# Optimization experiments

Measured on AMD Instinct MI355X. Metric: run time of the kernel, lower is better.

The kernel has to match this reference:

```python
import jax, jax.numpy as jnp
import numpy as np

NUM_AGENTS = 5
B = 512          # graphs in batch
NP = 50          # nodes per graph
N = B * NP
EPG = 400        # edges per graph
E = B * EPG
H, C = 8, 64     # heads, per-head channels
F = H * C        # 512 node feature dim after concat
GRU_IN = 2 * F   # agent emb + graph emb
GRU_H = 128


def _gat_layer(x, src, dst, ea, W, a_src, a_dst, We, ae, b):
    # PyG GATConv: per-edge additive attention with edge features, softmax over dst
    n = x.shape[0]
    h = (x @ W).reshape(n, H, C)                          # [n,H,C]
    al = (h * a_src).sum(-1)[src] + (h * a_dst).sum(-1)[dst] \
         + ((ea @ We).reshape(-1, H, C) * ae).sum(-1)     # [e,H]
    al = jax.nn.leaky_relu(al, 0.2)
    amax = jax.ops.segment_max(al, dst, num_segments=n)
    amax = jnp.where(jnp.isfinite(amax), amax, 0.0)
    p = jnp.exp(al - amax[dst])
    denom = jax.ops.segment_sum(p, dst, num_segments=n)
    alpha = p / (denom[dst] + 1e-16)
    out = jax.ops.segment_sum(alpha[:, :, None] * h[src], dst, num_segments=n)
    return out.reshape(n, F) + b


def _gru(x_seq, h0, Wih, Whh, bih, bhh):
    # torch nn.GRU math, batch_first input [B,T,I]
    def step(h, x_t):
        gi = x_t @ Wih + bih
        gh = h @ Whh + bhh
        ir, iz, inn = jnp.split(gi, 3, axis=-1)
        hr, hz, hn = jnp.split(gh, 3, axis=-1)
        r = jax.nn.sigmoid(ir + hr)
        z = jax.nn.sigmoid(iz + hz)
        n_ = jnp.tanh(inn + r * hn)
        h_new = (1.0 - z) * n_ + z * h
        return h_new, h_new
    h_last, ys = jax.lax.scan(step, h0, jnp.swapaxes(x_seq, 0, 1))
    return jnp.swapaxes(ys, 0, 1), h_last


def _forward(x, edge_index, edge_attr, hidden_state,
             W1, a_src1, a_dst1, We1, ae1, b1,
             W2, a_src2, a_dst2, We2, ae2, b2,
             W3, a_src3, a_dst3, We3, ae3, b3,
             gru_Wih, gru_Whh, gru_bih, gru_bhh,
             fc1_W, fc1_b, fc2_W, fc2_b, log_std):
    src, dst = edge_index[0], edge_index[1]
    # conv1: add_self_loops=False
    x1 = jax.nn.relu(_gat_layer(x, src, dst, edge_attr, W1, a_src1, a_dst1, We1, ae1, b1))
    # conv2/3: add self loops with fill_value='mean' (mean of incoming edge_attr per node)
    cnt = jax.ops.segment_sum(jnp.ones((E,), x.dtype), dst, num_segments=N)
    loop_attr = jax.ops.segment_sum(edge_attr, dst, num_segments=N) / jnp.maximum(cnt, 1.0)[:, None]
    loops = jnp.arange(N, dtype=edge_index.dtype)
    src2 = jnp.concatenate([src, loops])
    dst2 = jnp.concatenate([dst, loops])
    ea2 = jnp.concatenate([edge_attr, loop_attr], axis=0)
    x2 = jax.nn.relu(_gat_layer(x1, src2, dst2, ea2, W2, a_src2, a_dst2, We2, ae2, b2))
    x3 = jax.nn.relu(_gat_layer(x2, src2, dst2, ea2, W3, a_src3, a_dst3, We3, ae3, b3))
    # global mean pool (each graph has NP nodes, contiguous)
    batch = jnp.repeat(jnp.arange(B), NP)
    graph_emb = jax.ops.segment_sum(x3, batch, num_segments=B) / NP   # [B,F]
    # first NUM_AGENTS nodes of each graph
    agent_idx = (jnp.arange(B)[:, None] * NP + jnp.arange(NUM_AGENTS)).reshape(-1)
    agent_emb = x3[agent_idx]                                          # [B*A,F]
    graph_rep = jnp.repeat(graph_emb, NUM_AGENTS, axis=0)
    combined = jnp.concatenate([agent_emb, graph_rep], axis=1).reshape(B, NUM_AGENTS, GRU_IN)
    gru_out, h_last = _gru(combined, hidden_state[0], gru_Wih, gru_Whh, gru_bih, gru_bhh)
    f1 = jax.nn.relu(gru_out.reshape(-1, GRU_H) @ fc1_W + fc1_b)
    action_mean = (f1 @ fc2_W + fc2_b).reshape(B, NUM_AGENTS, -1)
    action_std = jnp.broadcast_to(jnp.exp(jnp.clip(log_std, -20.0, 2.0)), action_mean.shape)
    return action_mean, action_std, h_last[None]


def setup_inputs() -> dict:
    ks = jax.random.split(jax.random.key(0), 24)
    rng = np.random.default_rng(0)
    # random edges within each graph, no self-loops
    src_l = rng.integers(0, NP, size=(B, EPG))
    dst_l = (src_l + 1 + rng.integers(0, NP - 1, size=(B, EPG))) % NP
    off = (np.arange(B) * NP)[:, None]
    edge_index = jnp.asarray(np.stack([(src_l + off).reshape(-1), (dst_l + off).reshape(-1)]), dtype=jnp.int32)

    def p(k, shape, fan):
        return jax.random.normal(k, shape, jnp.float32) / float(np.sqrt(fan))

    z = lambda *s: jnp.zeros(s, jnp.float32)
    return {
        "x": jax.random.normal(ks[0], (N, 4), jnp.float32),
        "edge_index": edge_index,
        "edge_attr": jax.random.uniform(ks[1], (E, 1), jnp.float32),
        "hidden_state": z(1, B, GRU_H),
        "W1": p(ks[2], (4, F), 4), "a_src1": p(ks[3], (H, C), C), "a_dst1": p(ks[4], (H, C), C),
        "We1": p(ks[5], (1, F), 1), "ae1": p(ks[6], (H, C), C), "b1": z(F),
        "W2": p(ks[7], (F, F), F), "a_src2": p(ks[8], (H, C), C), "a_dst2": p(ks[9], (H, C), C),
        "We2": p(ks[10], (1, F), 1), "ae2": p(ks[11], (H, C), C), "b2": z(F),
        "W3": p(ks[12], (F, F), F), "a_src3": p(ks[13], (H, C), C), "a_dst3": p(ks[14], (H, C), C),
        "We3": p(ks[15], (1, F), 1), "ae3": p(ks[16], (H, C), C), "b3": z(F),
        "gru_Wih": p(ks[17], (GRU_IN, 3 * GRU_H), GRU_IN),
        "gru_Whh": p(ks[18], (GRU_H, 3 * GRU_H), GRU_H),
        "gru_bih": z(3 * GRU_H), "gru_bhh": z(3 * GRU_H),
        "fc1_W": p(ks[19], (GRU_H, 64), GRU_H), "fc1_b": z(64),
        "fc2_W": p(ks[20], (64, 3), 64), "fc2_b": z(3),
        "log_std": jnp.full((1, 1, 3), -1.6, jnp.float32),
    }


def reference(x, edge_index, edge_attr, hidden_state,
              W1, a_src1, a_dst1, We1, ae1, b1,
              W2, a_src2, a_dst2, We2, ae2, b2,
              W3, a_src3, a_dst3, We3, ae3, b3,
              gru_Wih, gru_Whh, gru_bih, gru_bhh,
              fc1_W, fc1_b, fc2_W, fc2_b, log_std):
    return _forward(x, edge_index, edge_attr, hidden_state,
                    W1, a_src1, a_dst1, We1, ae1, b1,
                    W2, a_src2, a_dst2, We2, ae2, b2,
                    W3, a_src3, a_dst3, We3, ae3, b3,
                    gru_Wih, gru_Whh, gru_bih, gru_bhh,
                    fc1_W, fc1_b, fc2_W, fc2_b, log_std)
```

## Files before the change

### kernel.cpp

```cpp
#include <hip/hip_runtime.h>
#include <math.h>

#define NN 25600
#define BB 512
#define NP 50
#define EPG 400
#define EE 204800
#define HH 8
#define CC 64
#define FF 512
#define GRUH 128
#define GRUIN 1024
#define NTP 25664

typedef unsigned short ushort_t;
typedef __attribute__((ext_vector_type(8))) short bf16x8;
typedef __attribute__((ext_vector_type(4))) float f32x4;

__device__ __forceinline__ float wave_reduce_sum(float v) {
  #pragma unroll
  for (int m = 32; m >= 1; m >>= 1) v += __shfl_xor(v, m, 64);
  return v;
}

__device__ __forceinline__ ushort_t f2bf(float x) {
  union { float f; unsigned int u; } v; v.f = x;
  unsigned int r = v.u + 0x7fffu + ((v.u >> 16) & 1u);
  return (ushort_t)(r >> 16);
}

__device__ __forceinline__ float bf2f(ushort_t u) {
  union { unsigned int u; float f; } v; v.u = ((unsigned int)u) << 16;
  return v.f;
}

__device__ __forceinline__ void gload_lds16(const ushort_t* g, ushort_t* l) {
  __builtin_amdgcn_global_load_lds(
      (const __attribute__((address_space(1))) void*)g,
      (__attribute__((address_space(3))) void*)l, 16, 0, 0);
}

__global__ void k_wedot(const float* __restrict__ We1, const float* __restrict__ ae1,
                        const float* __restrict__ We2, const float* __restrict__ ae2,
                        const float* __restrict__ We3, const float* __restrict__ ae3,
                        float* __restrict__ wdot) {
  const float* We = blockIdx.x == 0 ? We1 : (blockIdx.x == 1 ? We2 : We3);
  const float* ae = blockIdx.x == 0 ? ae1 : (blockIdx.x == 1 ? ae2 : ae3);
  int head = threadIdx.x >> 6, lane = threadIdx.x & 63;
  float v = We[head * 64 + lane] * ae[head * 64 + lane];
  v = wave_reduce_sum(v);
  if (lane == 0) wdot[blockIdx.x * 8 + head] = v;
}

__global__ void k_lattr(const int* __restrict__ ei, const float* __restrict__ eattr,
                        float* __restrict__ lattr, float* __restrict__ gmm) {
  int g = blockIdx.x, tid = threadIdx.x;
  __shared__ float esum[NP];
  __shared__ int cnt[NP];
  __shared__ unsigned int mn, mx;
  if (tid < NP) { esum[tid] = 0.f; cnt[tid] = 0; }
  if (tid == 0) { mn = 0x7f7fffffu; mx = 0u; }
  __syncthreads();
  for (int e = tid; e < EPG; e += 256) {
    int ge = g * EPG + e;
    int d = ei[EE + ge] - g * NP;
    float a = eattr[ge];
    atomicAdd(&esum[d], a);
    atomicAdd(&cnt[d], 1);
    atomicMax(&mx, __float_as_uint(a));
    atomicMin(&mn, __float_as_uint(a));
  }
  __syncthreads();
  if (tid < NP) {
    float la = esum[tid] / (float)max(cnt[tid], 1);
    lattr[g * NP + tid] = la;
    atomicMax(&mx, __float_as_uint(la));
    atomicMin(&mn, __float_as_uint(la));
  }
  __syncthreads();
  if (tid == 0) { gmm[g * 2] = __uint_as_float(mn); gmm[g * 2 + 1] = __uint_as_float(mx); }
}

__global__ __launch_bounds__(256) void k_cvt_t(const float* __restrict__ W,
                                               ushort_t* __restrict__ Wt,
                                               int K, int N) {
  __shared__ float t[32][33];
  int n0 = blockIdx.x * 32, k0 = blockIdx.y * 32;
  int tx = threadIdx.x & 31, ty = threadIdx.x >> 5;
  #pragma unroll
  for (int i = 0; i < 4; i++)
    t[ty + i * 8][tx] = W[(size_t)(k0 + ty + i * 8) * N + n0 + tx];
  __syncthreads();
  #pragma unroll
  for (int i = 0; i < 4; i++)
    Wt[(size_t)(n0 + ty + i * 8) * K + k0 + tx] = f2bf(t[tx][ty + i * 8]);
}

__global__ __launch_bounds__(256) void k_bgemmT(
    const ushort_t* __restrict__ Wt, const ushort_t* __restrict__ X,
    const float* __restrict__ a_src, const float* __restrict__ a_dst,
    ushort_t* __restrict__ hT, float* __restrict__ ssg, float* __restrict__ sdg) {
  __shared__ ushort_t As[128 * 32];
  __shared__ ushort_t Bs[128 * 32];
  int tid = threadIdx.x;
  int w = tid >> 6, l = tid & 63;
  int row0 = blockIdx.y * 128;
  int col0 = blockIdx.x * 128;
  int wr = w >> 1, wc = w & 1;

  f32x4 acc[4][4];
  #pragma unroll
  for (int i = 0; i < 4; i++)
    #pragma unroll
    for (int j = 0; j < 4; j++) acc[i][j] = (f32x4){0.f, 0.f, 0.f, 0.f};

  int srow = w * 32 + (l >> 2);
  int skcol = (l & 3) * 8;
  const ushort_t* Ag = Wt + (size_t)(row0 + srow) * FF + skcol;
  const ushort_t* Bg = X + (size_t)(col0 + srow) * FF + skcol;
  ushort_t* AsW = &As[w * 1024];
  ushort_t* BsW = &Bs[w * 1024];

  int m_l = l & 15, kq = (l >> 4) * 8;
  const ushort_t* ArdA = &As[(wr * 64 + m_l) * 32 + kq];
  const ushort_t* BrdB = &Bs[(wc * 64 + m_l) * 32 + kq];

  for (int k0 = 0; k0 < FF; k0 += 32) {
    gload_lds16(Ag + k0, AsW);
    gload_lds16(Ag + (size_t)16 * FF + k0, AsW + 512);
    gload_lds16(Bg + k0, BsW);
    gload_lds16(Bg + (size_t)16 * FF + k0, BsW + 512);
    __syncthreads();
    bf16x8 af[4], bfr[4];
    #pragma unroll
    for (int t = 0; t < 4; t++) {
      af[t]  = *(const bf16x8*)(ArdA + t * 16 * 32);
      bfr[t] = *(const bf16x8*)(BrdB + t * 16 * 32);
    }
    #pragma unroll
    for (int mt = 0; mt < 4; mt++)
      #pragma unroll
      for (int nt = 0; nt < 4; nt++)
        acc[mt][nt] = __builtin_amdgcn_mfma_f32_16x16x32_bf16(af[mt], bfr[nt], acc[mt][nt], 0, 0, 0);
    __syncthreads();
  }

  int head = (row0 + wr * 64) >> 6;
  int rq = (l >> 4) * 4, cl = l & 15;
  float ds[4] = {0.f, 0.f, 0.f, 0.f}, dd[4] = {0.f, 0.f, 0.f, 0.f};
  #pragma unroll
  for (int mt = 0; mt < 4; mt++) {
    #pragma unroll
    for (int r = 0; r < 4; r++) {
      int f = row0 + wr * 64 + mt * 16 + rq + r;
      float a_s = a_src[f], a_d = a_dst[f];
      #pragma unroll
      for (int nt = 0; nt < 4; nt++) {
        float v = acc[mt][nt][r];
        ds[nt] += v * a_s;
        dd[nt] += v * a_d;
        int n = col0 + wc * 64 + nt * 16 + cl;
        hT[(size_t)f * NTP + n] = f2bf(v);
      }
    }
  }
  #pragma unroll
  for (int nt = 0; nt < 4; nt++) {
    ds[nt] += __shfl_xor(ds[nt], 16, 64); ds[nt] += __shfl_xor(ds[nt], 32, 64);
    dd[nt] += __shfl_xor(dd[nt], 16, 64); dd[nt] += __shfl_xor(dd[nt], 32, 64);
  }
  if (l < 16) {
    #pragma unroll
    for (int nt = 0; nt < 4; nt++) {
      int n = col0 + wc * 64 + nt * 16 + l;
      ssg[(size_t)n * 8 + head] = ds[nt];
      sdg[(size_t)n * 8 + head] = dd[nt];
    }
  }
}

__global__ __launch_bounds__(256) void k_gatm(
    const ushort_t* __restrict__ hT,
    const float* __restrict__ xin, const float* __restrict__ W1,
    ushort_t* __restrict__ xout,
    const float* __restrict__ a_src, const float* __restrict__ a_dst,
    const float* __restrict__ ssg, const float* __restrict__ sdg,
    const int* __restrict__ ei, const float* __restrict__ eattr,
    const float* __restrict__ lattr, const float* __restrict__ gmm,
    const float* __restrict__ wdot_all, const float* __restrict__ bias,
    int layer, int self_loops) {
  int g = blockIdx.x, hd = blockIdx.y, tid = threadIdx.x;
  int w = tid >> 6, lane = tid & 63;
  const bool l1 = (W1 != nullptr);

  __shared__ __align__(16) ushort_t ht[64 * 72];
  __shared__ __align__(16) float P[50 * 68];
  __shared__ __align__(16) ushort_t Am[64 * 72];
  __shared__ __align__(16) ushort_t ab[16 * 72];
  __shared__ float ssl[64], sdl[64], lat[64];

  float wdot = wdot_all[layer * 8 + hd];
  float minEA = gmm[g * 2], maxEA = gmm[g * 2 + 1];
  float cmax = fmaxf(wdot * maxEA, wdot * minEA);
  if (tid < NP) lat[tid] = lattr[g * NP + tid];
  int m_l = lane & 15, kq8 = (lane >> 4) * 8;

  if (l1) {
    if (tid < 64) ab[tid] = f2bf(a_src[hd * 64 + tid]);
    else if (tid < 128) ab[72 + (tid - 64)] = f2bf(a_dst[hd * 64 + (tid - 64)]);
    { uint4* z = (uint4*)ht; uint4 zz = make_uint4(0u, 0u, 0u, 0u);
      for (int i = tid; i < 576; i += 256) z[i] = zz; }
    float w1c0 = W1[hd * 64 + lane], w1c1 = W1[512 + hd * 64 + lane],
          w1c2 = W1[1024 + hd * 64 + lane], w1c3 = W1[1536 + hd * 64 + lane];
    __syncthreads();
    ushort_t* hrow = (ushort_t*)P;
    #pragma unroll
    for (int i = 0; i < 13; i++) {
      int s = w + 4 * i;
      if (s < NP) {
        const float4 xv = *(const float4*)(xin + (size_t)(g * NP + s) * 4);
        float hv = xv.x * w1c0 + xv.y * w1c1 + xv.z * w1c2 + xv.w * w1c3;
        ushort_t hb = f2bf(hv);
        hrow[s * 72 + lane] = hb;
        ht[lane * 72 + (s ^ (lane & 56))] = hb;
      }
    }
    __syncthreads();
    { int s0 = w * 16;
      f32x4 dacc = (f32x4){0.f, 0.f, 0.f, 0.f};
      #pragma unroll
      for (int kc = 0; kc < 2; kc++) {
        bf16x8 a = *(const bf16x8*)(&ab[m_l * 72 + kc * 32 + kq8]);
        bf16x8 b = *(const bf16x8*)(&hrow[(s0 + m_l) * 72 + kc * 32 + kq8]);
        dacc = __builtin_amdgcn_mfma_f32_16x16x32_bf16(a, b, dacc, 0, 0, 0);
      }
      if (lane < 16) { ssl[s0 + lane] = dacc[0]; sdl[s0 + lane] = dacc[1]; }
    }
    __syncthreads();
    if (tid >= NP && tid < 64) { ssl[tid] = -1e30f; sdl[tid] = 0.f; }
  } else {
    for (int i = tid; i < 2048; i += 256) {
      int c = i >> 5, q = i & 31;
      *(unsigned int*)(&ht[c * 72 + q * 2]) =
          *(const unsigned int*)(&hT[(size_t)(hd * 64 + c) * NTP + g * NP + q * 2]);
    }
    if (tid < 64) {
      ssl[tid] = (tid < NP) ? ssg[(size_t)(g * NP + tid) * 8 + hd] : -1e30f;
      sdl[tid] = (tid < NP) ? sdg[(size_t)(g * NP + tid) * 8 + hd] : 0.f;
    }
  }
  { uint4* z = (uint4*)P; uint4 zz = make_uint4(0u, 0u, 0u, 0u);
    for (int i = tid; i < 850; i += 256) z[i] = zz; }
  __syncthreads();

  float mv = ssl[lane];
  #pragma unroll
  for (int m = 32; m >= 1; m >>= 1) mv = fmaxf(mv, __shfl_xor(mv, m, 64));

  for (int e = tid; e < EPG; e += 256) {
    int eg = g * EPG + e;
    int s = ei[eg] - g * NP;
    int d = ei[EE + eg] - g * NP;
    float al = ssl[s] + sdl[d] + eattr[eg] * wdot;
    al = al > 0.f ? al : 0.2f * al;
    float ub = mv + sdl[d] + cmax;
    ub = ub > 0.f ? ub : 0.2f * ub;
    atomicAdd(&P[d * 68 + s], __expf(al - ub));
  }
  if (self_loops && tid < NP) {
    int d = tid;
    float al = ssl[d] + sdl[d] + lat[d] * wdot;
    al = al > 0.f ? al : 0.2f * al;
    float ub = mv + sdl[d] + cmax;
    ub = ub > 0.f ? ub : 0.2f * ub;
    atomicAdd(&P[d * 68 + d], __expf(al - ub));
  }
  __syncthreads();

  { int d = tid >> 2, part = tid & 3;
    if (d < NP) {
      f32x4 v0 = *(const f32x4*)(&P[d * 68 + part * 16 + 0]);
      f32x4 v1 = *(const f32x4*)(&P[d * 68 + part * 16 + 4]);
      f32x4 v2 = *(const f32x4*)(&P[d * 68 + part * 16 + 8]);
      f32x4 v3 = *(const f32x4*)(&P[d * 68 + part * 16 + 12]);
      float sm = (v0[0] + v0[1] + v0[2] + v0[3]) + (v1[0] + v1[1] + v1[2] + v1[3])
               + (v2[0] + v2[1] + v2[2] + v2[3]) + (v3[0] + v3[1] + v3[2] + v3[3]);
      sm += __shfl_xor(sm, 1, 64);
      sm += __shfl_xor(sm, 2, 64);
      float inv = 1.f / (sm + 1e-16f);
      union { ushort_t u[8]; uint4 q; } p0, p1;
      p0.u[0] = f2bf(v0[0] * inv); p0.u[1] = f2bf(v0[1] * inv);
      p0.u[2] = f2bf(v0[2] * inv); p0.u[3] = f2bf(v0[3] * inv);
      p0.u[4] = f2bf(v1[0] * inv); p0.u[5] = f2bf(v1[1] * inv);
      p0.u[6] = f2bf(v1[2] * inv); p0.u[7] = f2bf(v1[3] * inv);
      p1.u[0] = f2bf(v2[0] * inv); p1.u[1] = f2bf(v2[1] * inv);
      p1.u[2] = f2bf(v2[2] * inv); p1.u[3] = f2bf(v2[3] * inv);
      p1.u[4] = f2bf(v3[0] * inv); p1.u[5] = f2bf(v3[1] * inv);
      p1.u[6] = f2bf(v3[2] * inv); p1.u[7] = f2bf(v3[3] * inv);
      *(uint4*)(&Am[d * 72 + part * 16]) = p0.q;
      *(uint4*)(&Am[d * 72 + part * 16 + 8]) = p1.q;
    } else {
      uint4 zz = make_uint4(0u, 0u, 0u, 0u);
      *(uint4*)(&Am[d * 72 + part * 16]) = zz;
      *(uint4*)(&Am[d * 72 + part * 16 + 8]) = zz;
    }
  }
  __syncthreads();

  int d0 = w * 16;
  f32x4 acc[4];
  #pragma unroll
  for (int ct = 0; ct < 4; ct++) acc[ct] = (f32x4){0.f, 0.f, 0.f, 0.f};
  #pragma unroll
  for (int kc = 0; kc < 2; kc++) {
    int kb = kc * 32 + kq8;
    bf16x8 bfrag = *(const bf16x8*)(&Am[(d0 + m_l) * 72 + kb]);
    #pragma unroll
    for (int ct = 0; ct < 4; ct++) {
      int m = ct * 16 + m_l;
      int ka = l1 ? (kb ^ (m & 56)) : kb;
      bf16x8 afrag = *(const bf16x8*)(&ht[m * 72 + ka]);
      acc[ct] = __builtin_amdgcn_mfma_f32_16x16x32_bf16(afrag, bfrag, acc[ct], 0, 0, 0);
    }
  }

  int d = d0 + m_l, rq = (lane >> 4) * 4;
  if (d < NP) {
    #pragma unroll
    for (int ct = 0; ct < 4; ct++) {
      int cb = ct * 16 + rq;
      const float4 bv = *(const float4*)(&bias[hd * 64 + cb]);
      union { ushort_t u[4]; uint2 v; } pk;
      pk.u[0] = f2bf(fmaxf(acc[ct][0] + bv.x, 0.f));
      pk.u[1] = f2bf(fmaxf(acc[ct][1] + bv.y, 0.f));
      pk.u[2] = f2bf(fmaxf(acc[ct][2] + bv.z, 0.f));
      pk.u[3] = f2bf(fmaxf(acc[ct][3] + bv.w, 0.f));
      *(uint2*)(&xout[(size_t)(g * NP + d) * FF + hd * 64 + cb]) = pk.v;
    }
  }
}

__global__ __launch_bounds__(256) void k_bgemm(
    const ushort_t* __restrict__ A, const ushort_t* __restrict__ Bt,
    const float* __restrict__ bias, float* __restrict__ C,
    int M, int N, int K) {
  __shared__ ushort_t As[128 * 32];
  __shared__ ushort_t Bs[128 * 32];
  int tid = threadIdx.x;
  int w = tid >> 6, l = tid & 63;
  int row0 = blockIdx.y * 128, col0 = blockIdx.x * 128;
  int wr = w >> 1, wc = w & 1;

  f32x4 acc[4][4];
  #pragma unroll
  for (int i = 0; i < 4; i++)
    #pragma unroll
    for (int j = 0; j < 4; j++) acc[i][j] = (f32x4){0.f, 0.f, 0.f, 0.f};

  int srow = w * 32 + (l >> 2);
  int skcol = (l & 3) * 8;
  const ushort_t* Ag = A + (size_t)(row0 + srow) * K + skcol;
  const ushort_t* Bg = Bt + (size_t)(col0 + srow) * K + skcol;
  ushort_t* AsW = &As[w * 1024];
  ushort_t* BsW = &Bs[w * 1024];

  int m_l = l & 15, kq = (l >> 4) * 8;
  const ushort_t* ArdA = &As[(wr * 64 + m_l) * 32 + kq];
  const ushort_t* BrdB = &Bs[(wc * 64 + m_l) * 32 + kq];

  for (int k0 = 0; k0 < K; k0 += 32) {
    gload_lds16(Ag + k0, AsW);
    gload_lds16(Ag + (size_t)16 * K + k0, AsW + 512);
    gload_lds16(Bg + k0, BsW);
    gload_lds16(Bg + (size_t)16 * K + k0, BsW + 512);
    __syncthreads();
    bf16x8 af[4], bfr[4];
    #pragma unroll
    for (int t = 0; t < 4; t++) {
      af[t]  = *(const bf16x8*)(ArdA + t * 16 * 32);
      bfr[t] = *(const bf16x8*)(BrdB + t * 16 * 32);
    }
    #pragma unroll
    for (int mt = 0; mt < 4; mt++)
      #pragma unroll
      for (int nt = 0; nt < 4; nt++)
        acc[mt][nt] = __builtin_amdgcn_mfma_f32_16x16x32_bf16(af[mt], bfr[nt], acc[mt][nt], 0, 0, 0);
    __syncthreads();
  }

  int cl = l & 15, rq = (l >> 4) * 4;
  #pragma unroll
  for (int mt = 0; mt < 4; mt++) {
    #pragma unroll
    for (int nt = 0; nt < 4; nt++) {
      int col = col0 + wc * 64 + nt * 16 + cl;
      float bv = bias ? bias[col] : 0.f;
      #pragma unroll
      for (int r = 0; r < 4; r++) {
        int row = row0 + wr * 64 + mt * 16 + rq + r;
        C[(size_t)row * N + col] = acc[mt][nt][r] + bv;
      }
    }
  }
}

__global__ void k_pool(const ushort_t* __restrict__ x3, ushort_t* __restrict__ combined) {
  int b = blockIdx.x, tid = threadIdx.x;
  float a0 = 0.f, a1 = 0.f;
  for (int n = 0; n < NP; n++) {
    const ushort_t* r = x3 + (size_t)(b * NP + n) * FF;
    a0 += bf2f(r[tid]); a1 += bf2f(r[tid + 256]);
  }
  a0 *= (1.f / NP); a1 *= (1.f / NP);
  ushort_t b0 = f2bf(a0), b1v = f2bf(a1);
  for (int t = 0; t < 5; t++) {
    ushort_t* cb = combined + (size_t)(b * 5 + t) * GRUIN;
    const ushort_t* ag = x3 + (size_t)(b * NP + t) * FF;
    cb[tid] = ag[tid];
    cb[tid + 256] = ag[tid + 256];
    cb[512 + tid] = b0;
    cb[768 + tid] = b1v;
  }
}

__global__ void k_gru(const float* __restrict__ gi_all, const float* __restrict__ h0,
                      const float* __restrict__ Whh, const float* __restrict__ bhh,
                      float* __restrict__ gru_out, float* __restrict__ hlast) {
  int b = blockIdx.x, tid = threadIdx.x;
  __shared__ float hl[GRUH];
  __shared__ float ghb[384];
  if (tid < GRUH) hl[tid] = h0[b * GRUH + tid];
  for (int t = 0; t < 5; t++) {
    __syncthreads();
    float acc = bhh[tid];
    for (int k = 0; k < GRUH; k++) acc += hl[k] * Whh[k * 384 + tid];
    ghb[tid] = acc;
    __syncthreads();
    if (tid < GRUH) {
      const float* gi = gi_all + (size_t)(b * 5 + t) * 384;
      float r = 1.f / (1.f + expf(-(gi[tid] + ghb[tid])));
      float z = 1.f / (1.f + expf(-(gi[128 + tid] + ghb[128 + tid])));
      float nn = tanhf(gi[256 + tid] + r * ghb[256 + tid]);
      float hn = (1.f - z) * nn + z * hl[tid];
      gru_out[(size_t)(b * 5 + t) * GRUH + tid] = hn;
      hl[tid] = hn;
    }
  }
  __syncthreads();
  if (tid < GRUH) hlast[b * GRUH + tid] = hl[tid];
}

__global__ void k_fc(const float* __restrict__ gru_out, const float* __restrict__ fc1W,
                     const float* __restrict__ fc1b, const float* __restrict__ fc2W,
                     const float* __restrict__ fc2b, const float* __restrict__ log_std,
                     float* __restrict__ dout) {
  int row = blockIdx.x, tid = threadIdx.x;
  __shared__ float gbuf[GRUH];
  __shared__ float f1[64];
  gbuf[tid] = gru_out[(size_t)row * GRUH + tid];
  gbuf[tid + 64] = gru_out[(size_t)row * GRUH + 64 + tid];
  __syncthreads();
  float acc = fc1b[tid];
  for (int k = 0; k < GRUH; k++) acc += gbuf[k] * fc1W[k * 64 + tid];
  f1[tid] = fmaxf(acc, 0.f);
  __syncthreads();
  if (tid < 3) {
    float o = fc2b[tid];
    for (int j = 0; j < 64; j++) o += f1[j] * fc2W[j * 3 + tid];
    dout[row * 3 + tid] = o;
    float ls = log_std[tid];
    ls = fminf(fmaxf(ls, -20.f), 2.f);
    dout[7680 + row * 3 + tid] = expf(ls);
  }
}

extern "C" void kernel_launch(void* const* d_in, const int* in_sizes, int n_in,
                              void* d_out, int out_size, void* d_ws, size_t ws_size,
                              hipStream_t stream) {
  const float* x      = (const float*)d_in[0];
  const int*   ei     = (const int*)d_in[1];
  const float* eattr  = (const float*)d_in[2];
  const float* hstate = (const float*)d_in[3];
  const float* W1  = (const float*)d_in[4];
  const float* as1 = (const float*)d_in[5];
  const float* ad1 = (const float*)d_in[6];
  const float* We1 = (const float*)d_in[7];
  const float* ae1 = (const float*)d_in[8];
  const float* b1  = (const float*)d_in[9];
  const float* W2  = (const float*)d_in[10];
  const float* as2 = (const float*)d_in[11];
  const float* ad2 = (const float*)d_in[12];
  const float* We2 = (const float*)d_in[13];
  const float* ae2 = (const float*)d_in[14];
  const float* b2  = (const float*)d_in[15];
  const float* W3  = (const float*)d_in[16];
  const float* as3 = (const float*)d_in[17];
  const float* ad3 = (const float*)d_in[18];
  const float* We3 = (const float*)d_in[19];
  const float* ae3 = (const float*)d_in[20];
  const float* b3  = (const float*)d_in[21];
  const float* Wih = (const float*)d_in[22];
  const float* Whh = (const float*)d_in[23];
  const float* bih = (const float*)d_in[24];
  const float* bhh = (const float*)d_in[25];
  const float* fc1W = (const float*)d_in[26];
  const float* fc1b = (const float*)d_in[27];
  const float* fc2W = (const float*)d_in[28];
  const float* fc2b = (const float*)d_in[29];
  const float* lstd = (const float*)d_in[30];

  float* ws = (float*)d_ws;
  ushort_t* xbf = (ushort_t*)ws;
  ushort_t* hT  = (ushort_t*)(ws + 6553600);
  float* p = ws + 6553600 + 6569984;
  float* ssg   = p;           p += 204800;
  float* sdg   = p;           p += 204800;
  float* lattr = p;           p += 25600;
  float* gmm   = p;           p += 1024;
  float* wdot  = p;           p += 32;
  ushort_t* w2t  = (ushort_t*)p;  p += 131072;
  ushort_t* w3t  = (ushort_t*)p;  p += 131072;
  ushort_t* wiht = (ushort_t*)p;  p += 196608;
  ushort_t* cbf  = (ushort_t*)p;  p += 1310720;
  float* gi_all  = p;         p += 983040;
  float* gru_out = p;         p += 327680;
  float* dout = (float*)d_out;

  k_wedot<<<3, 512, 0, stream>>>(We1, ae1, We2, ae2, We3, ae3, wdot);
  k_lattr<<<BB, 256, 0, stream>>>(ei, eattr, lattr, gmm);
  k_cvt_t<<<dim3(16, 16), 256, 0, stream>>>(W2, w2t, FF, FF);
  k_cvt_t<<<dim3(16, 16), 256, 0, stream>>>(W3, w3t, FF, FF);
  k_cvt_t<<<dim3(12, 32), 256, 0, stream>>>(Wih, wiht, GRUIN, 384);

  k_gatm<<<dim3(BB, HH), 256, 0, stream>>>(nullptr, x, W1, xbf, as1, ad1,
                                           nullptr, nullptr, ei, eattr,
                                           lattr, gmm, wdot, b1, 0, 0);
  k_bgemmT<<<dim3(200, 4), 256, 0, stream>>>(w2t, xbf, as2, ad2, hT, ssg, sdg);
  k_gatm<<<dim3(BB, HH), 256, 0, stream>>>(hT, nullptr, nullptr, xbf, nullptr, nullptr,
                                           ssg, sdg, ei, eattr,
                                           lattr, gmm, wdot, b2, 1, 1);
  k_bgemmT<<<dim3(200, 4), 256, 0, stream>>>(w3t, xbf, as3, ad3, hT, ssg, sdg);
  k_gatm<<<dim3(BB, HH), 256, 0, stream>>>(hT, nullptr, nullptr, xbf, nullptr, nullptr,
                                           ssg, sdg, ei, eattr,
                                           lattr, gmm, wdot, b3, 2, 1);

  k_pool<<<BB, 256, 0, stream>>>(xbf, cbf);
  k_bgemm<<<dim3(3, 20), 256, 0, stream>>>(cbf, wiht, bih, gi_all, 2560, 384, GRUIN);

  k_gru<<<BB, 384, 0, stream>>>(gi_all, hstate, Whh, bhh, gru_out, dout + 15360);
  k_fc<<<2560, 64, 0, stream>>>(gru_out, fc1W, fc1b, fc2W, fc2b, lstd, dout);
}
```

Baseline: 364.7 us.

## Fuse mean-pool and combine into last GAT layer; precompute layer-1 projection separately

The mean-pool and combine step (k_pool) is folded into the epilogue of the third GAT kernel. It sums node outputs per graph with wave shuffles and LDS, then writes the agent rows and the pooled mean straight into the GRU input buffer, so the x3 layer output is never written out and read back. Layer 1's tiny 4-dim projection and its attention scores move to a new k_h1T kernel. That kernel writes the transposed bf16 hT layout, and the attention scores come from W1·a vectors precomputed in k_wedot. This lets all three GAT launches share one code path without the swizzle and MFMA branch, at the cost of an extra launch and hT traffic for layer 1.

```diff
diff --git a/kernel.cpp b/kernel.cpp
--- a/kernel.cpp
+++ b/kernel.cpp
@@ -29,11 +29,6 @@
   return (ushort_t)(r >> 16);
 }
 
-__device__ __forceinline__ float bf2f(ushort_t u) {
-  union { unsigned int u; float f; } v; v.u = ((unsigned int)u) << 16;
-  return v.f;
-}
-
 __device__ __forceinline__ void gload_lds16(const ushort_t* g, ushort_t* l) {
   __builtin_amdgcn_global_load_lds(
       (const __attribute__((address_space(1))) void*)g,
@@ -43,13 +38,26 @@
 __global__ void k_wedot(const float* __restrict__ We1, const float* __restrict__ ae1,
                         const float* __restrict__ We2, const float* __restrict__ ae2,
                         const float* __restrict__ We3, const float* __restrict__ ae3,
-                        float* __restrict__ wdot) {
-  const float* We = blockIdx.x == 0 ? We1 : (blockIdx.x == 1 ? We2 : We3);
-  const float* ae = blockIdx.x == 0 ? ae1 : (blockIdx.x == 1 ? ae2 : ae3);
+                        const float* __restrict__ W1, const float* __restrict__ as1,
+                        const float* __restrict__ ad1,
+                        float* __restrict__ wdot, float* __restrict__ wa) {
   int head = threadIdx.x >> 6, lane = threadIdx.x & 63;
-  float v = We[head * 64 + lane] * ae[head * 64 + lane];
-  v = wave_reduce_sum(v);
-  if (lane == 0) wdot[blockIdx.x * 8 + head] = v;
+  if (blockIdx.x < 3) {
+    const float* We = blockIdx.x == 0 ? We1 : (blockIdx.x == 1 ? We2 : We3);
+    const float* ae = blockIdx.x == 0 ? ae1 : (blockIdx.x == 1 ? ae2 : ae3);
+    float v = We[head * 64 + lane] * ae[head * 64 + lane];
+    v = wave_reduce_sum(v);
+    if (lane == 0) wdot[blockIdx.x * 8 + head] = v;
+  } else {
+    float as = as1[head * 64 + lane], ad = ad1[head * 64 + lane];
+    #pragma unroll
+    for (int k = 0; k < 4; k++) {
+      float wv = W1[k * 512 + head * 64 + lane];
+      float s = wave_reduce_sum(wv * as);
+      float d = wave_reduce_sum(wv * ad);
+      if (lane == 0) { wa[k * 8 + head] = s; wa[32 + k * 8 + head] = d; }
+    }
+  }
 }
 
 __global__ void k_lattr(const int* __restrict__ ei, const float* __restrict__ eattr,
@@ -94,6 +102,31 @@
   #pragma unroll
   for (int i = 0; i < 4; i++)
     Wt[(size_t)(n0 + ty + i * 8) * K + k0 + tx] = f2bf(t[tx][ty + i * 8]);
+}
+
+__global__ __launch_bounds__(256) void k_h1T(
+    const float* __restrict__ x, const float* __restrict__ W1,
+    const float* __restrict__ wa, ushort_t* __restrict__ hT,
+    float* __restrict__ ssg, float* __restrict__ sdg) {
+  int hd = blockIdx.y, tid = threadIdx.x;
+  int n = blockIdx.x * 512 + tid * 2;
+  const float4 x0 = *(const float4*)(x + (size_t)n * 4);
+  const float4 x1 = *(const float4*)(x + (size_t)(n + 1) * 4);
+  float s0 = x0.x * wa[hd] + x0.y * wa[8 + hd] + x0.z * wa[16 + hd] + x0.w * wa[24 + hd];
+  float s1 = x1.x * wa[hd] + x1.y * wa[8 + hd] + x1.z * wa[16 + hd] + x1.w * wa[24 + hd];
+  float d0 = x0.x * wa[32 + hd] + x0.y * wa[40 + hd] + x0.z * wa[48 + hd] + x0.w * wa[56 + hd];
+  float d1 = x1.x * wa[32 + hd] + x1.y * wa[40 + hd] + x1.z * wa[48 + hd] + x1.w * wa[56 + hd];
+  ssg[(size_t)n * 8 + hd] = s0; ssg[(size_t)(n + 1) * 8 + hd] = s1;
+  sdg[(size_t)n * 8 + hd] = d0; sdg[(size_t)(n + 1) * 8 + hd] = d1;
+  #pragma unroll 4
+  for (int fi = 0; fi < 64; fi++) {
+    int f = hd * 64 + fi;
+    float w0 = W1[f], w1 = W1[512 + f], w2 = W1[1024 + f], w3 = W1[1536 + f];
+    float h0 = x0.x * w0 + x0.y * w1 + x0.z * w2 + x0.w * w3;
+    float h1 = x1.x * w0 + x1.y * w1 + x1.z * w2 + x1.w * w3;
+    unsigned int pk = (unsigned int)f2bf(h0) | ((unsigned int)f2bf(h1) << 16);
+    *(unsigned int*)(&hT[(size_t)f * NTP + n]) = pk;
+  }
 }
 
 __global__ __launch_bounds__(256) void k_bgemmT(
@@ -181,9 +214,8 @@
 
 __global__ __launch_bounds__(256) void k_gatm(
     const ushort_t* __restrict__ hT,
-    const float* __restrict__ xin, const float* __restrict__ W1,
     ushort_t* __restrict__ xout,
-    const float* __restrict__ a_src, const float* __restrict__ a_dst,
+    ushort_t* __restrict__ cbf,
     const float* __restrict__ ssg, const float* __restrict__ sdg,
     const int* __restrict__ ei, const float* __restrict__ eattr,
     const float* __restrict__ lattr, const float* __restrict__ gmm,
@@ -191,63 +223,26 @@
     int layer, int self_loops) {
   int g = blockIdx.x, hd = blockIdx.y, tid = threadIdx.x;
   int w = tid >> 6, lane = tid & 63;
-  const bool l1 = (W1 != nullptr);
 
   __shared__ __align__(16) ushort_t ht[64 * 72];
   __shared__ __align__(16) float P[50 * 68];
   __shared__ __align__(16) ushort_t Am[64 * 72];
-  __shared__ __align__(16) ushort_t ab[16 * 72];
-  __shared__ float ssl[64], sdl[64], lat[64];
+  __shared__ float ssl[64], sdl[64];
+  __shared__ float gsum[4 * 64];
 
   float wdot = wdot_all[layer * 8 + hd];
   float minEA = gmm[g * 2], maxEA = gmm[g * 2 + 1];
   float cmax = fmaxf(wdot * maxEA, wdot * minEA);
-  if (tid < NP) lat[tid] = lattr[g * NP + tid];
   int m_l = lane & 15, kq8 = (lane >> 4) * 8;
 
-  if (l1) {
-    if (tid < 64) ab[tid] = f2bf(a_src[hd * 64 + tid]);
-    else if (tid < 128) ab[72 + (tid - 64)] = f2bf(a_dst[hd * 64 + (tid - 64)]);
-    { uint4* z = (uint4*)ht; uint4 zz = make_uint4(0u, 0u, 0u, 0u);
-      for (int i = tid; i < 576; i += 256) z[i] = zz; }
-    float w1c0 = W1[hd * 64 + lane], w1c1 = W1[512 + hd * 64 + lane],
-          w1c2 = W1[1024 + hd * 64 + lane], w1c3 = W1[1536 + hd * 64 + lane];
-    __syncthreads();
-    ushort_t* hrow = (ushort_t*)P;
-    #pragma unroll
-    for (int i = 0; i < 13; i++) {
-      int s = w + 4 * i;
-      if (s < NP) {
-        const float4 xv = *(const float4*)(xin + (size_t)(g * NP + s) * 4);
-        float hv = xv.x * w1c0 + xv.y * w1c1 + xv.z * w1c2 + xv.w * w1c3;
-        ushort_t hb = f2bf(hv);
-        hrow[s * 72 + lane] = hb;
-        ht[lane * 72 + (s ^ (lane & 56))] = hb;
-      }
-    }
-    __syncthreads();
-    { int s0 = w * 16;
-      f32x4 dacc = (f32x4){0.f, 0.f, 0.f, 0.f};
-      #pragma unroll
-      for (int kc = 0; kc < 2; kc++) {
-        bf16x8 a = *(const bf16x8*)(&ab[m_l * 72 + kc * 32 + kq8]);
-        bf16x8 b = *(const bf16x8*)(&hrow[(s0 + m_l) * 72 + kc * 32 + kq8]);
-        dacc = __builtin_amdgcn_mfma_f32_16x16x32_bf16(a, b, dacc, 0, 0, 0);
-      }
-      if (lane < 16) { ssl[s0 + lane] = dacc[0]; sdl[s0 + lane] = dacc[1]; }
-    }
-    __syncthreads();
-    if (tid >= NP && tid < 64) { ssl[tid] = -1e30f; sdl[tid] = 0.f; }
-  } else {
-    for (int i = tid; i < 2048; i += 256) {
-      int c = i >> 5, q = i & 31;
-      *(unsigned int*)(&ht[c * 72 + q * 2]) =
-          *(const unsigned int*)(&hT[(size_t)(hd * 64 + c) * NTP + g * NP + q * 2]);
-    }
-    if (tid < 64) {
-      ssl[tid] = (tid < NP) ? ssg[(size_t)(g * NP + tid) * 8 + hd] : -1e30f;
-      sdl[tid] = (tid < NP) ? sdg[(size_t)(g * NP + tid) * 8 + hd] : 0.f;
-    }
+  for (int i = tid; i < 2048; i += 256) {
+    int c = i >> 5, q = i & 31;
+    *(unsigned int*)(&ht[c * 72 + q * 2]) =
+        *(const unsigned int*)(&hT[(size_t)(hd * 64 + c) * NTP + g * NP + q * 2]);
+  }
+  if (tid < 64) {
+    ssl[tid] = (tid < NP) ? ssg[(size_t)(g * NP + tid) * 8 + hd] : -1e30f;
+    sdl[tid] = (tid < NP) ? sdg[(size_t)(g * NP + tid) * 8 + hd] : 0.f;
   }
   { uint4* z = (uint4*)P; uint4 zz = make_uint4(0u, 0u, 0u, 0u);
     for (int i = tid; i < 850; i += 256) z[i] = zz; }
@@ -269,7 +264,7 @@
   }
   if (self_loops && tid < NP) {
     int d = tid;
-    float al = ssl[d] + sdl[d] + lat[d] * wdot;
+    float al = ssl[d] + sdl[d] + lattr[g * NP + d] * wdot;
     al = al > 0.f ? al : 0.2f * al;
     float ub = mv + sdl[d] + cmax;
     ub = ub > 0.f ? ub : 0.2f * ub;
@@ -317,25 +312,60 @@
     bf16x8 bfrag = *(const bf16x8*)(&Am[(d0 + m_l) * 72 + kb]);
     #pragma unroll
     for (int ct = 0; ct < 4; ct++) {
-      int m = ct * 16 + m_l;
-      int ka = l1 ? (kb ^ (m & 56)) : kb;
-      bf16x8 afrag = *(const bf16x8*)(&ht[m * 72 + ka]);
+      bf16x8 afrag = *(const bf16x8*)(&ht[(ct * 16 + m_l) * 72 + kb]);
       acc[ct] = __builtin_amdgcn_mfma_f32_16x16x32_bf16(afrag, bfrag, acc[ct], 0, 0, 0);
     }
   }
 
   int d = d0 + m_l, rq = (lane >> 4) * 4;
-  if (d < NP) {
+  bool valid = (d < NP);
+  float vv[4][4];
+  #pragma unroll
+  for (int ct = 0; ct < 4; ct++) {
+    const float4 bv = *(const float4*)(&bias[hd * 64 + ct * 16 + rq]);
+    vv[ct][0] = fmaxf(acc[ct][0] + bv.x, 0.f);
+    vv[ct][1] = fmaxf(acc[ct][1] + bv.y, 0.f);
+    vv[ct][2] = fmaxf(acc[ct][2] + bv.z, 0.f);
+    vv[ct][3] = fmaxf(acc[ct][3] + bv.w, 0.f);
+  }
+
+  if (cbf == nullptr) {
+    if (valid) {
+      #pragma unroll
+      for (int ct = 0; ct < 4; ct++) {
+        union { ushort_t u[4]; uint2 v; } pk;
+        pk.u[0] = f2bf(vv[ct][0]); pk.u[1] = f2bf(vv[ct][1]);
+        pk.u[2] = f2bf(vv[ct][2]); pk.u[3] = f2bf(vv[ct][3]);
+        *(uint2*)(&xout[(size_t)(g * NP + d) * FF + hd * 64 + ct * 16 + rq]) = pk.v;
+      }
+    }
+  } else {
     #pragma unroll
     for (int ct = 0; ct < 4; ct++) {
-      int cb = ct * 16 + rq;
-      const float4 bv = *(const float4*)(&bias[hd * 64 + cb]);
-      union { ushort_t u[4]; uint2 v; } pk;
-      pk.u[0] = f2bf(fmaxf(acc[ct][0] + bv.x, 0.f));
-      pk.u[1] = f2bf(fmaxf(acc[ct][1] + bv.y, 0.f));
-      pk.u[2] = f2bf(fmaxf(acc[ct][2] + bv.z, 0.f));
-      pk.u[3] = f2bf(fmaxf(acc[ct][3] + bv.w, 0.f));
-      *(uint2*)(&xout[(size_t)(g * NP + d) * FF + hd * 64 + cb]) = pk.v;
+      #pragma unroll
+      for (int r = 0; r < 4; r++) {
+        float t = valid ? vv[ct][r] : 0.f;
+        t += __shfl_xor(t, 1, 64); t += __shfl_xor(t, 2, 64);
+        t += __shfl_xor(t, 4, 64); t += __shfl_xor(t, 8, 64);
+        if (m_l == 0) gsum[w * 64 + ct * 16 + rq + r] = t;
+      }
+    }
+    if (w == 0 && m_l < 5) {
+      #pragma unroll
+      for (int ct = 0; ct < 4; ct++) {
+        union { ushort_t u[4]; uint2 v; } pk;
+        pk.u[0] = f2bf(vv[ct][0]); pk.u[1] = f2bf(vv[ct][1]);
+        pk.u[2] = f2bf(vv[ct][2]); pk.u[3] = f2bf(vv[ct][3]);
+        *(uint2*)(&cbf[(size_t)(g * 5 + d) * GRUIN + hd * 64 + ct * 16 + rq]) = pk.v;
+      }
+    }
+    __syncthreads();
+    if (tid < 64) {
+      float mean = (gsum[tid] + gsum[64 + tid] + gsum[128 + tid] + gsum[192 + tid]) * (1.f / NP);
+      ushort_t mb = f2bf(mean);
+      #pragma unroll
+      for (int t = 0; t < 5; t++)
+        cbf[(size_t)(g * 5 + t) * GRUIN + 512 + hd * 64 + tid] = mb;
     }
   }
 }
@@ -401,25 +431,6 @@
         C[(size_t)row * N + col] = acc[mt][nt][r] + bv;
       }
     }
-  }
-}
-
-__global__ void k_pool(const ushort_t* __restrict__ x3, ushort_t* __restrict__ combined) {
-  int b = blockIdx.x, tid = threadIdx.x;
-  float a0 = 0.f, a1 = 0.f;
-  for (int n = 0; n < NP; n++) {
-    const ushort_t* r = x3 + (size_t)(b * NP + n) * FF;
-    a0 += bf2f(r[tid]); a1 += bf2f(r[tid + 256]);
-  }
-  a0 *= (1.f / NP); a1 *= (1.f / NP);
-  ushort_t b0 = f2bf(a0), b1v = f2bf(a1);
-  for (int t = 0; t < 5; t++) {
-    ushort_t* cb = combined + (size_t)(b * 5 + t) * GRUIN;
-    const ushort_t* ag = x3 + (size_t)(b * NP + t) * FF;
-    cb[tid] = ag[tid];
-    cb[tid + 256] = ag[tid + 256];
-    cb[512 + tid] = b0;
-    cb[768 + tid] = b1v;
   }
 }
 
@@ -518,6 +529,7 @@
   float* lattr = p;           p += 25600;
   float* gmm   = p;           p += 1024;
   float* wdot  = p;           p += 32;
+  float* wa    = p;           p += 64;
   ushort_t* w2t  = (ushort_t*)p;  p += 131072;
   ushort_t* w3t  = (ushort_t*)p;  p += 131072;
   ushort_t* wiht = (ushort_t*)p;  p += 196608;
@@ -526,25 +538,22 @@
   float* gru_out = p;         p += 327680;
   float* dout = (float*)d_out;
 
-  k_wedot<<<3, 512, 0, stream>>>(We1, ae1, We2, ae2, We3, ae3, wdot);
+  k_wedot<<<4, 512, 0, stream>>>(We1, ae1, We2, ae2, We3, ae3, W1, as1, ad1, wdot, wa);
   k_lattr<<<BB, 256, 0, stream>>>(ei, eattr, lattr, gmm);
   k_cvt_t<<<dim3(16, 16), 256, 0, stream>>>(W2, w2t, FF, FF);
   k_cvt_t<<<dim3(16, 16), 256, 0, stream>>>(W3, w3t, FF, FF);
   k_cvt_t<<<dim3(12, 32), 256, 0, stream>>>(Wih, wiht, GRUIN, 384);
 
-  k_gatm<<<dim3(BB, HH), 256, 0, stream>>>(nullptr, x, W1, xbf, as1, ad1,
-                                           nullptr, nullptr, ei, eattr,
+  k_h1T<<<dim3(50, 8), 256, 0, stream>>>(x, W1, wa, hT, ssg, sdg);
+  k_gatm<<<dim3(BB, HH), 256, 0, stream>>>(hT, xbf, nullptr, ssg, sdg, ei, eattr,
                                            lattr, gmm, wdot, b1, 0, 0);
   k_bgemmT<<<dim3(200, 4), 256, 0, stream>>>(w2t, xbf, as2, ad2, hT, ssg, sdg);
-  k_gatm<<<dim3(BB, HH), 256, 0, stream>>>(hT, nullptr, nullptr, xbf, nullptr, nullptr,
-                                           ssg, sdg, ei, eattr,
+  k_gatm<<<dim3(BB, HH), 256, 0, stream>>>(hT, xbf, nullptr, ssg, sdg, ei, eattr,
                                            lattr, gmm, wdot, b2, 1, 1);
   k_bgemmT<<<dim3(200, 4), 256, 0, stream>>>(w3t, xbf, as3, ad3, hT, ssg, sdg);
-  k_gatm<<<dim3(BB, HH), 256, 0, stream>>>(hT, nullptr, nullptr, xbf, nullptr, nullptr,
-                                           ssg, sdg, ei, eattr,
+  k_gatm<<<dim3(BB, HH), 256, 0, stream>>>(hT, nullptr, cbf, ssg, sdg, ei, eattr,
                                            lattr, gmm, wdot, b3, 2, 1);
 
-  k_pool<<<BB, 256, 0, stream>>>(xbf, cbf);
   k_bgemm<<<dim3(3, 20), 256, 0, stream>>>(cbf, wiht, bih, gi_all, 2560, 384, GRUIN);
 
   k_gru<<<BB, 384, 0, stream>>>(gi_all, hstate, Whh, bhh, gru_out, dout + 15360);
```

Result: slower. 379.2 us (+4.0%).
